# Kernel tuning notes

Measured on AMD Instinct MI355X. Metric: run time of the kernel, lower is better.

The kernel has to match this reference:

```python
import jax, jax.numpy as jnp
import numpy as np

# Standard JPEG luminance quantization table (quality 50)
_QTABLE = np.array([
    [16, 11, 10, 16, 24, 40, 51, 61],
    [12, 12, 14, 19, 26, 58, 60, 55],
    [14, 13, 16, 24, 40, 57, 69, 56],
    [14, 17, 22, 29, 51, 87, 80, 62],
    [18, 22, 37, 56, 68, 109, 103, 77],
    [24, 35, 55, 64, 81, 104, 113, 92],
    [49, 64, 78, 87, 103, 121, 120, 101],
    [72, 92, 95, 98, 112, 100, 103, 99]], dtype=np.float32)

def _dct_mtx(n=8):
    # Orthonormal DCT-II basis matrix: mtx @ block @ mtx.T is the 2-D DCT,
    # so mtx.T @ coeffs @ mtx is the inverse DCT used by this module.
    k = np.arange(n)[:, None]
    j = np.arange(n)[None, :]
    m = np.cos(np.pi * (2 * j + 1) * k / (2 * n)) * np.sqrt(2.0 / n)
    m[0, :] /= np.sqrt(2.0)
    return m.astype(np.float32)

def setup_inputs() -> dict:
    key = jax.random.key(0)
    B, C, H, W = 32, 1, 1024, 1024  # square image required by the reshape chain
    x = jax.random.normal(key, (B, C, H, W), dtype=jnp.float32) * 10.0
    return {
        "x": x,
        "qtable": jnp.asarray(_QTABLE),
        "mtx": jnp.asarray(_dct_mtx(8)),
    }

def reference(x, qtable, mtx):
    B, D1, D2, D3 = x.shape
    # view -> permute -> reshape chain extracting 8x8 blocks (faithful to torch code)
    y = x.reshape(B, D1 * D2 // 8, 8, D3)
    y = jnp.transpose(y, (0, 1, 3, 2))                       # (B, D1*D2/8, D3, 8)
    y = y.reshape(B, D1 * D2 * D3 // 64, 8, 8)
    y = jnp.transpose(y, (0, 1, 3, 2))                       # (B, Nblk, 8, 8)
    y = y * qtable                                           # dequantize
    # mtx.T @ y @ mtx  (batched tiny 8x8 IDCT)
    y = jnp.einsum('ji,bnjk,kl->bnil', mtx, y, mtx)
    # inverse reshape/permute chain back to image layout
    y = jnp.transpose(y, (0, 1, 3, 2))
    y = y.reshape(B, D1 * D2 // 8, D2, 8)
    y = jnp.transpose(y, (0, 1, 3, 2))
    return y.reshape(x.shape) + 128.0
```

## Files before the change

### kernel.cpp

```cpp
#include <hip/hip_runtime.h>


__global__ __launch_bounds__(256, 8) void bidct_kernel(
    const float* __restrict__ x, const float* __restrict__ qt,
    const float* __restrict__ mtx, float* __restrict__ out)
{
    const int n   = blockIdx.x * 256 + threadIdx.x;
    const int b   = n >> 3;
    const int i   = n & 7;
    const int img = b >> 14;
    const int m   = b & 16383;
    const int br  = m >> 7;
    const int bc  = m & 127;
    const size_t base = ((size_t)img << 20) + ((size_t)br << 13) + ((size_t)bc << 3);

    float mcol[8];
#pragma unroll
    for (int j = 0; j < 8; ++j) mcol[j] = mtx[j * 8 + i];

    const float* __restrict__ px = x + base;

    float T[8] = {0.f, 0.f, 0.f, 0.f, 0.f, 0.f, 0.f, 0.f};
#pragma unroll
    for (int jh = 0; jh < 2; ++jh) {
        float4 xa[4], xb[4];
#pragma unroll
        for (int jj = 0; jj < 4; ++jj) {
            const float* row = px + (size_t)(jh * 4 + jj) * 1024;
            xa[jj] = *reinterpret_cast<const float4*>(row);
            xb[jj] = *reinterpret_cast<const float4*>(row + 4);
        }
#pragma unroll
        for (int jj = 0; jj < 4; ++jj) {
            const int j = jh * 4 + jj;
            const float mj = mcol[j];
            T[0] = fmaf(mj, xa[jj].x * qt[j * 8 + 0], T[0]);
            T[1] = fmaf(mj, xa[jj].y * qt[j * 8 + 1], T[1]);
            T[2] = fmaf(mj, xa[jj].z * qt[j * 8 + 2], T[2]);
            T[3] = fmaf(mj, xa[jj].w * qt[j * 8 + 3], T[3]);
            T[4] = fmaf(mj, xb[jj].x * qt[j * 8 + 4], T[4]);
            T[5] = fmaf(mj, xb[jj].y * qt[j * 8 + 5], T[5]);
            T[6] = fmaf(mj, xb[jj].z * qt[j * 8 + 6], T[6]);
            T[7] = fmaf(mj, xb[jj].w * qt[j * 8 + 7], T[7]);
        }
    }

    float o[8] = {128.f, 128.f, 128.f, 128.f, 128.f, 128.f, 128.f, 128.f};
#pragma unroll
    for (int k = 0; k < 8; ++k) {
        const float tk = T[k];
#pragma unroll
        for (int l = 0; l < 8; ++l)
            o[l] = fmaf(tk, mtx[k * 8 + l], o[l]);
    }

    float* row = out + base + (size_t)i * 1024;
    *reinterpret_cast<float4*>(row)     = make_float4(o[0], o[1], o[2], o[3]);
    *reinterpret_cast<float4*>(row + 4) = make_float4(o[4], o[5], o[6], o[7]);
}

extern "C" void kernel_launch(void* const* d_in, const int* in_sizes, int n_in,
                              void* d_out, int out_size, void* d_ws, size_t ws_size,
                              hipStream_t stream) {
    const float* x   = (const float*)d_in[0];
    const float* qt  = (const float*)d_in[1];
    const float* mtx = (const float*)d_in[2];
    float*       out = (float*)d_out;

    const int grid = out_size / 2048;
    bidct_kernel<<<grid, 256, 0, stream>>>(x, qt, mtx, out);
}
```

Measured before the change: 240.7 us.

## Stage 8x64 wave tiles through LDS for coalesced loads and stores

Each wavefront now handles eight adjacent 8x8 blocks (an 8-row by 64-column strip). It loads the strip into padded shared memory with fully coalesced float4 accesses, computes the IDCT from LDS, writes results back into the same LDS tile, and stores them coalesced. This replaces the old per-thread strided row loads and stores, which touched 32-byte segments across many rows. It adds LDS traffic and relies on wave-synchronous execution with no __syncthreads between the LDS write and read phases.

```diff
diff --git a/kernel.cpp b/kernel.cpp
--- a/kernel.cpp
+++ b/kernel.cpp
@@ -5,44 +5,49 @@
     const float* __restrict__ x, const float* __restrict__ qt,
     const float* __restrict__ mtx, float* __restrict__ out)
 {
-    const int n   = blockIdx.x * 256 + threadIdx.x;
-    const int b   = n >> 3;
-    const int i   = n & 7;
-    const int img = b >> 14;
-    const int m   = b & 16383;
-    const int br  = m >> 7;
-    const int bc  = m & 127;
-    const size_t base = ((size_t)img << 20) + ((size_t)br << 13) + ((size_t)bc << 3);
+    __shared__ float4 tile4[4][136];
+
+    const int wv = threadIdx.x >> 6;
+    const int l  = threadIdx.x & 63;
+    float4* __restrict__ tw = tile4[wv];
+
+    const int wid  = blockIdx.x * 4 + wv;
+    const int img  = wid >> 11;
+    const int rest = wid & 2047;
+    const int rg   = rest >> 4;
+    const int cg   = rest & 15;
+    const size_t base = ((size_t)img << 20) + ((size_t)rg << 13) + ((size_t)cg << 6);
+
+#pragma unroll
+    for (int r = 0; r < 2; ++r) {
+        const int f  = r * 64 + l;
+        const int j  = f >> 4;
+        const int c4 = f & 15;
+        const float4 v = *reinterpret_cast<const float4*>(x + base + j * 1024 + c4 * 4);
+        tw[j * 17 + c4] = v;
+    }
+
+    const int bl = l >> 3;
+    const int i  = l & 7;
 
     float mcol[8];
 #pragma unroll
     for (int j = 0; j < 8; ++j) mcol[j] = mtx[j * 8 + i];
 
-    const float* __restrict__ px = x + base;
-
     float T[8] = {0.f, 0.f, 0.f, 0.f, 0.f, 0.f, 0.f, 0.f};
 #pragma unroll
-    for (int jh = 0; jh < 2; ++jh) {
-        float4 xa[4], xb[4];
-#pragma unroll
-        for (int jj = 0; jj < 4; ++jj) {
-            const float* row = px + (size_t)(jh * 4 + jj) * 1024;
-            xa[jj] = *reinterpret_cast<const float4*>(row);
-            xb[jj] = *reinterpret_cast<const float4*>(row + 4);
-        }
-#pragma unroll
-        for (int jj = 0; jj < 4; ++jj) {
-            const int j = jh * 4 + jj;
-            const float mj = mcol[j];
-            T[0] = fmaf(mj, xa[jj].x * qt[j * 8 + 0], T[0]);
-            T[1] = fmaf(mj, xa[jj].y * qt[j * 8 + 1], T[1]);
-            T[2] = fmaf(mj, xa[jj].z * qt[j * 8 + 2], T[2]);
-            T[3] = fmaf(mj, xa[jj].w * qt[j * 8 + 3], T[3]);
-            T[4] = fmaf(mj, xb[jj].x * qt[j * 8 + 4], T[4]);
-            T[5] = fmaf(mj, xb[jj].y * qt[j * 8 + 5], T[5]);
-            T[6] = fmaf(mj, xb[jj].z * qt[j * 8 + 6], T[6]);
-            T[7] = fmaf(mj, xb[jj].w * qt[j * 8 + 7], T[7]);
-        }
+    for (int j = 0; j < 8; ++j) {
+        const float4 xa = tw[j * 17 + bl * 2];
+        const float4 xb = tw[j * 17 + bl * 2 + 1];
+        const float mj = mcol[j];
+        T[0] = fmaf(mj, xa.x * qt[j * 8 + 0], T[0]);
+        T[1] = fmaf(mj, xa.y * qt[j * 8 + 1], T[1]);
+        T[2] = fmaf(mj, xa.z * qt[j * 8 + 2], T[2]);
+        T[3] = fmaf(mj, xa.w * qt[j * 8 + 3], T[3]);
+        T[4] = fmaf(mj, xb.x * qt[j * 8 + 4], T[4]);
+        T[5] = fmaf(mj, xb.y * qt[j * 8 + 5], T[5]);
+        T[6] = fmaf(mj, xb.z * qt[j * 8 + 6], T[6]);
+        T[7] = fmaf(mj, xb.w * qt[j * 8 + 7], T[7]);
     }
 
     float o[8] = {128.f, 128.f, 128.f, 128.f, 128.f, 128.f, 128.f, 128.f};
@@ -50,13 +55,20 @@
     for (int k = 0; k < 8; ++k) {
         const float tk = T[k];
 #pragma unroll
-        for (int l = 0; l < 8; ++l)
-            o[l] = fmaf(tk, mtx[k * 8 + l], o[l]);
+        for (int lcol = 0; lcol < 8; ++lcol)
+            o[lcol] = fmaf(tk, mtx[k * 8 + lcol], o[lcol]);
     }
 
-    float* row = out + base + (size_t)i * 1024;
-    *reinterpret_cast<float4*>(row)     = make_float4(o[0], o[1], o[2], o[3]);
-    *reinterpret_cast<float4*>(row + 4) = make_float4(o[4], o[5], o[6], o[7]);
+    tw[i * 17 + bl * 2]     = make_float4(o[0], o[1], o[2], o[3]);
+    tw[i * 17 + bl * 2 + 1] = make_float4(o[4], o[5], o[6], o[7]);
+
+#pragma unroll
+    for (int r = 0; r < 2; ++r) {
+        const int f  = r * 64 + l;
+        const int j  = f >> 4;
+        const int c4 = f & 15;
+        *reinterpret_cast<float4*>(out + base + j * 1024 + c4 * 4) = tw[j * 17 + c4];
+    }
 }
 
 extern "C" void kernel_launch(void* const* d_in, const int* in_sizes, int n_in,
```

After: 231.1 us. 4.0% less time.
